# Optimization experiments

Hardware: AMD Instinct MI355X
Metric: run time of the kernel (lower is better)

## Reference

```python
import jax, jax.numpy as jnp
import numpy as np

K = 6
N_LEVELS = [200000, 50000, 12500]
CHANNELS = [3, 64, 128, 256]
DEGREE = 32
FANIN = 4          # each pooled node averages FANIN fine nodes (D values = 1/FANIN)
NUM_CLASSES = 10


def setup_inputs() -> dict:
    key = jax.random.key(0)
    ks = jax.random.split(key, 16)
    inp = {}
    inp["x"] = jax.random.normal(ks[0], (N_LEVELS[0], 3), dtype=jnp.float32)
    # random sparse connectivity per level (edge lists, COO)
    for i, n in enumerate(N_LEVELS):
        inp[f"edge_index{i}"] = jax.random.randint(ks[1 + i], (2, n * DEGREE), 0, n)
    # sparse downscale matrices: row r of D_i averages FANIN source nodes
    inp["pool_cols0"] = jax.random.randint(ks[4], (N_LEVELS[1] * FANIN,), 0, N_LEVELS[0])
    inp["pool_cols1"] = jax.random.randint(ks[5], (N_LEVELS[2] * FANIN,), 0, N_LEVELS[1])
    # ChebConv parameters: weight [K, in, out] (Glorot-ish), bias [out]
    for i in range(3):
        cin, cout = CHANNELS[i], CHANNELS[i + 1]
        scale = (2.0 / (cin + cout)) ** 0.5
        inp[f"w{i}"] = scale * jax.random.normal(ks[6 + 2 * i], (K, cin, cout), dtype=jnp.float32)
        inp[f"b{i}"] = jnp.zeros((cout,), dtype=jnp.float32)
    lin_in = N_LEVELS[-1] * CHANNELS[-1]
    inp["lw"] = jax.random.normal(ks[12], (NUM_CLASSES, lin_in), dtype=jnp.float32) * (1.0 / np.sqrt(lin_in))
    inp["lb"] = jnp.zeros((NUM_CLASSES,), dtype=jnp.float32)
    return inp


def cheb_conv(x, edge_index, weight, bias):
    """PyG ChebConv, sym normalization, lambda_max=2, unit edge weights.
    Scaled Laplacian reduces to L_hat = -D^{-1/2} A D^{-1/2} (zero diagonal)."""
    row, col = edge_index[0], edge_index[1]
    n = x.shape[0]
    w = (row != col).astype(x.dtype)                 # remove_self_loops
    deg = jax.ops.segment_sum(w, row, num_segments=n)
    dinv = jnp.where(deg > 0, jax.lax.rsqrt(deg), 0.0)
    norm = -w * dinv[row] * dinv[col]                # [E]

    def prop(h):  # scatter-add of norm * gathered source features
        return jax.ops.segment_sum(norm[:, None] * h[col], row, num_segments=n)

    Tx0 = x
    out = Tx0 @ weight[0]
    Tx1 = prop(x)
    out = out + Tx1 @ weight[1]
    for k in range(2, weight.shape[0]):
        Tx2 = 2.0 * prop(Tx1) - Tx0
        out = out + Tx2 @ weight[k]
        Tx0, Tx1 = Tx1, Tx2
    return out + bias


def pool(x, cols, n_out):
    # sparse.mm(D, x) with D having FANIN entries of 1/FANIN per row (rows sorted)
    return x[cols].reshape(n_out, FANIN, x.shape[1]).mean(axis=1)


def reference(x, edge_index0, edge_index1, edge_index2, pool_cols0, pool_cols1,
              w0, b0, w1, b1, w2, b2, lw, lb):
    h = jax.nn.relu(cheb_conv(x, edge_index0, w0, b0))
    h = pool(h, pool_cols0, N_LEVELS[1])
    h = jax.nn.relu(cheb_conv(h, edge_index1, w1, b1))
    h = pool(h, pool_cols1, N_LEVELS[2])
    h = cheb_conv(h, edge_index2, w2, b2)
    return lw @ h.reshape(-1) + lb   # F.linear on flattened features -> [num_classes]
```

## Files before the change

### kernel.cpp

```cpp
#include <hip/hip_runtime.h>
#include <hip/hip_bf16.h>


#define N0 200000
#define N1 50000
#define N2 12500
#define KCH 6
#define NCLS 10

#define SB 8
#define BROWS 256
#define BCAP 10240
#define NBUK_MAX 800
#define NBLK 1024
#define TILE_MAX 6250
#define EMAX 6400000

typedef __hip_bfloat16 bf16;
typedef _Float16 f16;
typedef f16 f16x2 __attribute__((ext_vector_type(2)));
typedef f16 f16x4 __attribute__((ext_vector_type(4)));
typedef f16 f16x8 __attribute__((ext_vector_type(8)));
typedef float f32x4 __attribute__((ext_vector_type(4)));

static __device__ __forceinline__ float b2f(bf16 v) { return __bfloat162float(v); }
static __device__ __forceinline__ float blo(unsigned u) { return __uint_as_float(u << 16); }
static __device__ __forceinline__ float bhi(unsigned u) { return __uint_as_float(u & 0xFFFF0000u); }

__global__ void detect_k(const unsigned int* __restrict__ xb, int* __restrict__ flag) {
    __shared__ int cs;
    int t = threadIdx.x;
    if (t == 0) cs = 0;
    __syncthreads();
    unsigned w = xb[t];
    unsigned e = (w >> 7) & 0xFFu;
    if (e >= 0x30u && e <= 0x43u) atomicAdd(&cs, 1);
    __syncthreads();
    if (t == 0) flag[0] = (cs < 128) ? 1 : 0;
}

__global__ __launch_bounds__(256) void convw_k(const void* __restrict__ W, f16* __restrict__ wT,
                                               int Kd, int N, const int* __restrict__ flag) {
    int isf = flag[0];
    int idx = blockIdx.x * 256 + threadIdx.x;
    if (idx >= Kd * N) return;
    int n2 = idx / Kd, k = idx - n2 * Kd;
    float v;
    if (isf) v = ((const float*)W)[(size_t)k * N + n2];
    else     v = b2f(((const bf16*)W)[(size_t)k * N + n2]);
    wT[idx] = (f16)v;
}


__global__ __launch_bounds__(256) void binH_k(const int* __restrict__ rows, const int* __restrict__ cols,
                                              int* __restrict__ cntBB, int nbuk, int E, int tile) {
    __shared__ int cnt[NBUK_MAX];
    int t = threadIdx.x;
    for (int i = t; i < nbuk; i += 256) cnt[i] = 0;
    __syncthreads();
    int beg = blockIdx.x * tile;
    int end = beg + tile;
    if (end > E) end = E;
    for (int idx = beg + t; idx < end; idx += 256) {
        int r = rows[idx], c = cols[idx];
        if (r != c) atomicAdd(&cnt[r >> SB], 1);
    }
    __syncthreads();
    for (int i = t; i < nbuk; i += 256) cntBB[(size_t)blockIdx.x * nbuk + i] = cnt[i];
}

__global__ __launch_bounds__(256) void scanBB_k(int* __restrict__ cntBB, int* __restrict__ btot, int nbuk) {
    __shared__ int ps[256];
    int b = blockIdx.x, t = threadIdx.x;
    int vals[4];
    int pt = 0;
#pragma unroll
    for (int i = 0; i < 4; ++i) { vals[i] = cntBB[(size_t)(4 * t + i) * nbuk + b]; pt += vals[i]; }
    ps[t] = pt;
    __syncthreads();
    for (int off = 1; off < 256; off <<= 1) {
        int x = (t >= off) ? ps[t - off] : 0;
        __syncthreads();
        ps[t] += x;
        __syncthreads();
    }
    int ex = ps[t] - pt;
#pragma unroll
    for (int i = 0; i < 4; ++i) { cntBB[(size_t)(4 * t + i) * nbuk + b] = ex; ex += vals[i]; }
    if (t == 255) btot[b] = ps[255];
}

__global__ __launch_bounds__(1024) void scanb_k(const int* __restrict__ btot, int* __restrict__ bbase,
                                                int nbuk, int* __restrict__ ptr, int n) {
    __shared__ int s[1024];
    int t = threadIdx.x;
    int v = (t < nbuk) ? btot[t] : 0;
    s[t] = v;
    __syncthreads();
    for (int off = 1; off < 1024; off <<= 1) {
        int x = (t >= off) ? s[t - off] : 0;
        __syncthreads();
        s[t] += x;
        __syncthreads();
    }
    if (t < nbuk) bbase[t] = s[t] - v;
    if (t == 1023) ptr[n] = s[1023];
}

__global__ __launch_bounds__(256) void binS_k(const int* __restrict__ rows, const int* __restrict__ cols,
                                              const int* __restrict__ cntBB, const int* __restrict__ bbase,
                                              unsigned* __restrict__ colB, int nbuk, int E, int tile) {
    __shared__ int lcnt[NBUK_MAX];
    __shared__ int lexc[NBUK_MAX];
    __shared__ int lfill[NBUK_MAX];
    __shared__ int gstart[NBUK_MAX];
    __shared__ int ps[256];
    __shared__ unsigned scol[TILE_MAX];
    int t = threadIdx.x;
    for (int i = t; i < nbuk; i += 256) { lcnt[i] = 0; lfill[i] = 0; }
    __syncthreads();
    int beg = blockIdx.x * tile;
    int end = beg + tile;
    if (end > E) end = E;
    for (int idx = beg + t; idx < end; idx += 256) {
        int r = rows[idx], c = cols[idx];
        if (r != c) atomicAdd(&lcnt[r >> SB], 1);
    }
    __syncthreads();
    int idx4 = 4 * t;
    int c4[4];
#pragma unroll
    for (int i = 0; i < 4; ++i) c4[i] = (idx4 + i < nbuk) ? lcnt[idx4 + i] : 0;
    int tot = c4[0] + c4[1] + c4[2] + c4[3];
    ps[t] = tot;
    __syncthreads();
    for (int off = 1; off < 256; off <<= 1) {
        int x = (t >= off) ? ps[t - off] : 0;
        __syncthreads();
        ps[t] += x;
        __syncthreads();
    }
    int run = ps[t] - tot;
#pragma unroll
    for (int i = 0; i < 4; ++i) {
        if (idx4 + i < nbuk) lexc[idx4 + i] = run;
        run += c4[i];
    }
    for (int i = t; i < nbuk; i += 256) gstart[i] = bbase[i] + cntBB[(size_t)blockIdx.x * nbuk + i];
    __syncthreads();
    for (int idx = beg + t; idx < end; idx += 256) {
        int r = rows[idx], c = cols[idx];
        if (r != c) {
            int b = r >> SB;
            int s = atomicAdd(&lfill[b], 1);
            scol[lexc[b] + s] = ((unsigned)(r & (BROWS - 1)) << 18) | (unsigned)c;
        }
    }
    __syncthreads();
    int wv = t >> 6, lane = t & 63;
    for (int b = wv; b < nbuk; b += 4) {
        int cnt2 = lcnt[b];
        int lsrc = lexc[b], gdst = gstart[b];
        for (int i = lane; i < cnt2; i += 64) colB[gdst + i] = scol[lsrc + i];
    }
}

__global__ __launch_bounds__(256) void binB_k(const int* __restrict__ btot, const int* __restrict__ bbase,
                                              const unsigned* __restrict__ colB,
                                              int* __restrict__ ptr, float* __restrict__ dinv,
                                              int* __restrict__ colS, int n) {
    __shared__ int lcnt[BROWS];
    __shared__ int lexc[BROWS];
    __shared__ int lfill[BROWS];
    __shared__ int scol[BCAP];
    int b = blockIdx.x;
    int t = threadIdx.x;
    int rowbase = b << SB;
    int rowend = rowbase + BROWS;
    if (rowend > n) rowend = n;
    int nrows = rowend - rowbase;
    int count = btot[b];
    int base = bbase[b];
    const unsigned* slab = colB + base;
    lcnt[t] = 0;
    __syncthreads();
    for (int i = t; i < count; i += 256) atomicAdd(&lcnt[slab[i] >> 18], 1);
    __syncthreads();
    int v = lcnt[t];
    lexc[t] = v;
    __syncthreads();
    for (int off = 1; off < 256; off <<= 1) {
        int x = (t >= off) ? lexc[t - off] : 0;
        __syncthreads();
        lexc[t] += x;
        __syncthreads();
    }
    int excl = lexc[t] - v;
    __syncthreads();
    lexc[t] = excl;
    __syncthreads();
    if (t < nrows) {
        ptr[rowbase + t] = base + excl;
        dinv[rowbase + t] = (v > 0) ? rsqrtf((float)v) : 0.f;
    }
    int nh = (count <= BCAP) ? 1 : 2;
    int rspan = BROWS / nh;
    for (int h = 0; h < nh; ++h) {
        int rowLo = h * rspan, rowHi = rowLo + rspan;
        int segOff = lexc[rowLo];
        int segEnd = (rowHi >= BROWS) ? count : lexc[rowHi];
        int segCnt = segEnd - segOff;
        lfill[t] = 0;
        __syncthreads();
        for (int i = t; i < count; i += 256) {
            unsigned pk = slab[i];
            int rl = pk >> 18;
            if (rl >= rowLo && rl < rowHi) {
                int s = atomicAdd(&lfill[rl], 1);
                scol[lexc[rl] + s - segOff] = (int)(pk & 0x3FFFFu);
            }
        }
        __syncthreads();
        for (int i = t; i < segCnt; i += 256) colS[base + segOff + i] = scol[i];
        __syncthreads();
    }
}


__global__ __launch_bounds__(256) void convert_x_k(const void* __restrict__ x, f16* __restrict__ Tx,
                                                   f16x4* __restrict__ G0,
                                                   const float* __restrict__ dinv, int n,
                                                   const int* __restrict__ flag) {
    int isf = flag[0];
    int r = blockIdx.x * 256 + threadIdx.x;
    if (r >= n) return;
    float v0, v1, v2;
    if (isf) {
        const float* xf = (const float*)x;
        v0 = xf[3 * r]; v1 = xf[3 * r + 1]; v2 = xf[3 * r + 2];
    } else {
        const bf16* xh = (const bf16*)x;
        v0 = b2f(xh[3 * r]); v1 = b2f(xh[3 * r + 1]); v2 = b2f(xh[3 * r + 2]);
    }
    f16x4 pk = {(f16)v0, (f16)v1, (f16)v2, (f16)dinv[r]};
    *(f16x4*)(Tx + (size_t)r * 24) = pk;
    G0[r] = pk;
}


__global__ __launch_bounds__(256) void prop_narrow_k(const int* __restrict__ ptr, const int* __restrict__ colS,
                                                     const float* __restrict__ dinv,
                                                     const f16x4* __restrict__ gin, f16x4* __restrict__ gout,
                                                     f16* __restrict__ oslot,
                                                     int n, float alpha, int useSub) {
    int wv = threadIdx.x >> 6, half = (threadIdx.x >> 5) & 1, sl = threadIdx.x & 31;
    int r = blockIdx.x * 8 + wv * 2 + half;
    if (r >= n) return;
    int s = ptr[r], e = ptr[r + 1];
    float dr = dinv[r];
    float a0 = 0.f, a1 = 0.f, a2 = 0.f;
    for (int idx = s + sl; idx < e; idx += 32) {
        int c = colS[idx];
        f16x4 h = gin[c];
        float nrm = -dr * (float)h.w;
        a0 += nrm * (float)h.x;
        a1 += nrm * (float)h.y;
        a2 += nrm * (float)h.z;
    }
#pragma unroll
    for (int off2 = 16; off2 > 0; off2 >>= 1) {
        a0 += __shfl_xor(a0, off2);
        a1 += __shfl_xor(a1, off2);
        a2 += __shfl_xor(a2, off2);
    }
    if (sl == 0) {
        float v0 = alpha * a0, v1 = alpha * a1, v2 = alpha * a2;
        if (useSub) {
            f16x4 sv = gout[r];
            v0 -= (float)sv.x; v1 -= (float)sv.y; v2 -= (float)sv.z;
        }
        f16x4 ov = {(f16)v0, (f16)v1, (f16)v2, (f16)dr};
        gout[r] = ov;
        *(f16x4*)(oslot + (size_t)r * 24) = ov;
    }
}

__global__ __launch_bounds__(256) void prop_wide2_k(const int* __restrict__ ptr, const int* __restrict__ colS,
                                                    const float* __restrict__ dinv, const f16* __restrict__ hin,
                                                    const f16* __restrict__ sub, f16* __restrict__ o,
                                                    int ld, int n, float alpha, int useSub) {
    int wv = threadIdx.x >> 6, lane = threadIdx.x & 63;
    int p = lane >> 5, q = lane & 31;
    int r = blockIdx.x * 4 + wv;
    if (r >= n) return;
    int s = ptr[r], e = ptr[r + 1];
    float dr = dinv[r];
    float ax = 0.f, ay = 0.f;
    for (int base = s; base < e; base += 64) {
        int idx = base + lane;
        int c = 0;
        float dc = 0.f;
        if (idx < e) { c = colS[idx]; dc = dinv[c]; }
        int cnt2 = e - base;
        if (cnt2 > 64) cnt2 = 64;
        int j = 0;
        for (; j + 4 <= cnt2; j += 4) {
            int j0 = j + p, j1 = j + 2 + p;
            int c0 = __shfl(c, j0), c1 = __shfl(c, j1);
            float n0 = -dr * __shfl(dc, j0), n1 = -dr * __shfl(dc, j1);
            f16x2 h0 = *(const f16x2*)(hin + (size_t)c0 * ld + 2 * q);
            f16x2 h1 = *(const f16x2*)(hin + (size_t)c1 * ld + 2 * q);
            ax += n0 * (float)h0.x + n1 * (float)h1.x;
            ay += n0 * (float)h0.y + n1 * (float)h1.y;
        }
        for (; j < cnt2; j += 2) {
            int jj = j + p;
            int valid = jj < cnt2;
            int cc = __shfl(c, valid ? jj : 0);
            float nd = __shfl(dc, valid ? jj : 0);
            float nrm = valid ? -dr * nd : 0.f;
            f16x2 h = *(const f16x2*)(hin + (size_t)cc * ld + 2 * q);
            ax += nrm * (float)h.x;
            ay += nrm * (float)h.y;
        }
    }
    ax += __shfl_xor(ax, 32);
    ay += __shfl_xor(ay, 32);
    if (p == 0) {
        size_t rb = (size_t)r * ld + 2 * q;
        float vx = alpha * ax, vy = alpha * ay;
        if (useSub) {
            f16x2 sv = *(const f16x2*)(sub + rb);
            vx -= (float)sv.x; vy -= (float)sv.y;
        }
        f16x2 ov = {(f16)vx, (f16)vy};
        *(f16x2*)(o + rb) = ov;
    }
}

__global__ __launch_bounds__(256) void prop_wide1h_k(const int* __restrict__ ptr, const int* __restrict__ colS,
                                                     const float* __restrict__ dinv, const f16* __restrict__ hin,
                                                     const f16* __restrict__ sub, f16* __restrict__ o,
                                                     int ld, int n, float alpha, int useSub) {
    int wv = threadIdx.x >> 6, lane = threadIdx.x & 63;
    int r = blockIdx.x * 4 + wv;
    if (r >= n) return;
    int s = ptr[r], e = ptr[r + 1];
    float dr = dinv[r];
    float ax = 0.f, ay = 0.f;
    for (int base = s; base < e; base += 64) {
        int idx = base + lane;
        int c = 0;
        float dc = 0.f;
        if (idx < e) { c = colS[idx]; dc = dinv[c]; }
        int cnt2 = e - base;
        if (cnt2 > 64) cnt2 = 64;
        int j = 0;
        for (; j + 4 <= cnt2; j += 4) {
            int c0 = __shfl(c, j), c1 = __shfl(c, j + 1), c2 = __shfl(c, j + 2), c3 = __shfl(c, j + 3);
            float n0 = -dr * __shfl(dc, j), n1 = -dr * __shfl(dc, j + 1);
            float n2 = -dr * __shfl(dc, j + 2), n3 = -dr * __shfl(dc, j + 3);
            f16x2 h0 = *(const f16x2*)(hin + (size_t)c0 * ld + 2 * lane);
            f16x2 h1 = *(const f16x2*)(hin + (size_t)c1 * ld + 2 * lane);
            f16x2 h2 = *(const f16x2*)(hin + (size_t)c2 * ld + 2 * lane);
            f16x2 h3 = *(const f16x2*)(hin + (size_t)c3 * ld + 2 * lane);
            ax += n0 * (float)h0.x + n1 * (float)h1.x + n2 * (float)h2.x + n3 * (float)h3.x;
            ay += n0 * (float)h0.y + n1 * (float)h1.y + n2 * (float)h2.y + n3 * (float)h3.y;
        }
        for (; j < cnt2; ++j) {
            int cc = __shfl(c, j);
            float nrm = -dr * __shfl(dc, j);
            f16x2 h = *(const f16x2*)(hin + (size_t)cc * ld + 2 * lane);
            ax += nrm * (float)h.x;
            ay += nrm * (float)h.y;
        }
    }
    size_t rb = (size_t)r * ld + 2 * lane;
    float vx = alpha * ax, vy = alpha * ay;
    if (useSub) {
        f16x2 sv = *(const f16x2*)(sub + rb);
        vx -= (float)sv.x; vy -= (float)sv.y;
    }
    f16x2 ov = {(f16)vx, (f16)vy};
    *(f16x2*)(o + rb) = ov;
}


__global__ __launch_bounds__(256) void gemm_mfma2_k(const f16* __restrict__ A, int lda,
                                                    const f16* __restrict__ WT,
                                                    const void* __restrict__ bias,
                                                    float* __restrict__ C, int M, int N, int K, int flags,
                                                    const int* __restrict__ flag) {
    __shared__ f16 As[64][40];
    __shared__ f16 Bs[64][40];
    int isf = flag[0];
    int t = threadIdx.x;
    int w = t >> 6, l = t & 63, q = l >> 4, m16 = l & 15;
    int m0 = blockIdx.y * 64, n0 = blockIdx.x * 64;
    f32x4 acc[4] = {};
    for (int k0 = 0; k0 < K; k0 += 32) {
        {
            int row = t >> 2, cg = (t & 3) * 8;
            int gm = m0 + row;
            f16x8 av = {};
            if (gm < M) av = *(const f16x8*)(A + (size_t)gm * lda + k0 + cg);
            *(f16x8*)&As[row][cg] = av;
        }
        {
            int nr = t >> 2, cg = (t & 3) * 8;
            f16x8 bv = *(const f16x8*)(WT + (size_t)(n0 + nr) * K + k0 + cg);
            *(f16x8*)&Bs[nr][cg] = bv;
        }
        __syncthreads();
        f16x8 a = *(const f16x8*)&As[w * 16 + m16][q * 8];
        f16x8 b0 = *(const f16x8*)&Bs[m16][q * 8];
        f16x8 b1 = *(const f16x8*)&Bs[16 + m16][q * 8];
        f16x8 b2 = *(const f16x8*)&Bs[32 + m16][q * 8];
        f16x8 b3 = *(const f16x8*)&Bs[48 + m16][q * 8];
        acc[0] = __builtin_amdgcn_mfma_f32_16x16x32_f16(a, b0, acc[0], 0, 0, 0);
        acc[1] = __builtin_amdgcn_mfma_f32_16x16x32_f16(a, b1, acc[1], 0, 0, 0);
        acc[2] = __builtin_amdgcn_mfma_f32_16x16x32_f16(a, b2, acc[2], 0, 0, 0);
        acc[3] = __builtin_amdgcn_mfma_f32_16x16x32_f16(a, b3, acc[3], 0, 0, 0);
        __syncthreads();
    }
#pragma unroll
    for (int tile = 0; tile < 4; ++tile) {
        int gn = n0 + tile * 16 + m16;
        float bv = 0.f;
        if (flags & 4) {
            if (isf) bv = ((const float*)bias)[gn];
            else     bv = b2f(((const bf16*)bias)[gn]);
        }
#pragma unroll
        for (int i = 0; i < 4; ++i) {
            int gm = m0 + w * 16 + q * 4 + i;
            if (gm < M) {
                float v = acc[tile][i] + bv;
                if (flags & 1) v = fmaxf(v, 0.f);
                C[(size_t)gm * N + gn] = v;
            }
        }
    }
}


__global__ __launch_bounds__(256) void gemm_k(const f16* __restrict__ A, int lda,
                                              const void* __restrict__ W,
                                              const void* __restrict__ bias,
                                              float* __restrict__ C, int M, int N, int K, int flags,
                                              const int* __restrict__ flag) {
    __shared__ float As[16][65];
    __shared__ float Ws[16][64];
    int isf = flag[0];
    int pack3 = flags & 8;
    int t = threadIdx.x;
    int tn = t & 15, tm = t >> 4;
    int m0 = blockIdx.y * 64, n0 = blockIdx.x * 64;
    float acc[4][4] = {};
    for (int k0 = 0; k0 < K; k0 += 16) {
#pragma unroll
        for (int i = 0; i < 4; ++i) {
            int idx = i * 256 + t;
            int m = idx >> 4, k = idx & 15;
            int gm = m0 + m, gk = k0 + k;
            int phys = pack3 ? (gk + gk / 3) : gk;
            As[k][m] = (gm < M && gk < K) ? (float)A[(size_t)gm * lda + phys] : 0.f;
        }
        if (isf) {
            const float* Wf = (const float*)W;
#pragma unroll
            for (int i = 0; i < 4; ++i) {
                int idx = i * 256 + t;
                int k = idx >> 6, nn = idx & 63;
                int gk = k0 + k;
                Ws[k][nn] = (gk < K) ? Wf[(size_t)gk * N + n0 + nn] : 0.f;
            }
        } else {
            const bf16* Wh = (const bf16*)W;
#pragma unroll
            for (int i = 0; i < 4; ++i) {
                int idx = i * 256 + t;
                int k = idx >> 6, nn = idx & 63;
                int gk = k0 + k;
                Ws[k][nn] = (gk < K) ? b2f(Wh[(size_t)gk * N + n0 + nn]) : 0.f;
            }
        }
        __syncthreads();
#pragma unroll
        for (int kk = 0; kk < 16; ++kk) {
            float a[4], b[4];
#pragma unroll
            for (int i = 0; i < 4; ++i) a[i] = As[kk][tm * 4 + i];
#pragma unroll
            for (int j = 0; j < 4; ++j) b[j] = Ws[kk][tn * 4 + j];
#pragma unroll
            for (int i = 0; i < 4; ++i)
#pragma unroll
                for (int j = 0; j < 4; ++j) acc[i][j] += a[i] * b[j];
        }
        __syncthreads();
    }
#pragma unroll
    for (int i = 0; i < 4; ++i) {
        int gm = m0 + tm * 4 + i;
        if (gm >= M) continue;
#pragma unroll
        for (int j = 0; j < 4; ++j) {
            int gn = n0 + tn * 4 + j;
            size_t ci = (size_t)gm * N + gn;
            float v = acc[i][j];
            if (flags & 4) {
                if (isf) v += ((const float*)bias)[gn];
                else     v += b2f(((const bf16*)bias)[gn]);
            }
            if (flags & 1) v = fmaxf(v, 0.f);
            C[ci] = v;
        }
    }
}


__global__ __launch_bounds__(256) void pool_k(const float* __restrict__ in, const int* __restrict__ pcols,
                                              f16* __restrict__ out, int n_out, int C, int ld) {
    int idx = blockIdx.x * 256 + threadIdx.x;
    if (idx >= n_out * C) return;
    int r = idx / C, ch = idx - r * C;
    const int* pc = pcols + (size_t)r * 4;
    float ssum = 0.f;
#pragma unroll
    for (int f = 0; f < 4; ++f) ssum += in[(size_t)pc[f] * C + ch];
    out[(size_t)r * ld + ch] = (f16)(0.25f * ssum);
}


__global__ __launch_bounds__(256) void linear10b_k(const float* __restrict__ h, const void* __restrict__ lw,
                                                   float* __restrict__ accum, int LIN, const int* __restrict__ flag) {
    int isf = flag[0];
    int t = threadIdx.x;
    int nvec = LIN >> 3;
    int stride = gridDim.x * 256;
    float p[NCLS];
#pragma unroll
    for (int c = 0; c < NCLS; ++c) p[c] = 0.f;
    const float4* h4 = (const float4*)h;
    if (isf) {
        const float4* lw4 = (const float4*)lw;
        size_t ro = (size_t)(LIN >> 2);
        for (int i = blockIdx.x * 256 + t; i < nvec; i += stride) {
            float4 a0 = h4[2 * i], a1 = h4[2 * i + 1];
#pragma unroll
            for (int c = 0; c < NCLS; ++c) {
                float4 b0v = lw4[c * ro + 2 * i], b1v = lw4[c * ro + 2 * i + 1];
                p[c] += a0.x * b0v.x + a0.y * b0v.y + a0.z * b0v.z + a0.w * b0v.w
                      + a1.x * b1v.x + a1.y * b1v.y + a1.z * b1v.z + a1.w * b1v.w;
            }
        }
    } else {
        const uint4* lwv = (const uint4*)lw;
        size_t ro = (size_t)nvec;
        for (int i = blockIdx.x * 256 + t; i < nvec; i += stride) {
            float4 a0 = h4[2 * i], a1 = h4[2 * i + 1];
#pragma unroll
            for (int c = 0; c < NCLS; ++c) {
                uint4 w4 = lwv[c * ro + i];
                p[c] += a0.x * blo(w4.x) + a0.y * bhi(w4.x)
                      + a0.z * blo(w4.y) + a0.w * bhi(w4.y)
                      + a1.x * blo(w4.z) + a1.y * bhi(w4.z)
                      + a1.z * blo(w4.w) + a1.w * bhi(w4.w);
            }
        }
    }
    __shared__ float wsum[4][NCLS];
    int wv = t >> 6, lane = t & 63;
#pragma unroll
    for (int c = 0; c < NCLS; ++c) {
        float v = p[c];
        for (int off2 = 32; off2 > 0; off2 >>= 1) v += __shfl_down(v, off2);
        if (lane == 0) wsum[wv][c] = v;
    }
    __syncthreads();
    if (t < NCLS) {
        float s = wsum[0][t] + wsum[1][t] + wsum[2][t] + wsum[3][t];
        unsafeAtomicAdd(&accum[t], s);
    }
}

__global__ void finalize_k(const float* __restrict__ accum, const void* __restrict__ lb,
                           void* __restrict__ outp, const int* __restrict__ flag) {
    int isf = flag[0];
    int t = threadIdx.x;
    if (t < NCLS) {
        float lbv;
        if (isf) lbv = ((const float*)lb)[t];
        else     lbv = b2f(((const bf16*)lb)[t]);
        float v = accum[t] + lbv;
        if (isf) ((float*)outp)[t] = v;
        else     ((bf16*)outp)[t] = __float2bfloat16(v);
    }
}

__global__ void diag_k(void* __restrict__ outp, float val, const int* __restrict__ flag) {
    int isf = flag[0];
    int t = threadIdx.x;
    if (t < NCLS) {
        if (isf) ((float*)outp)[t] = val;
        else     ((bf16*)outp)[t] = __float2bfloat16(val);
    }
}


extern "C" void kernel_launch(void* const* d_in, const int* in_sizes, int n_in,
                              void* d_out, int out_size, void* d_ws, size_t ws_size,
                              hipStream_t stream) {
    const void* x  = d_in[0];
    const int* ei0 = (const int*)d_in[1];
    const int* ei1 = (const int*)d_in[2];
    const int* ei2 = (const int*)d_in[3];
    const int* pc0 = (const int*)d_in[4];
    const int* pc1 = (const int*)d_in[5];
    const void* w0 = d_in[6];
    const void* b0 = d_in[7];
    const void* w1 = d_in[8];
    const void* b1 = d_in[9];
    const void* w2 = d_in[10];
    const void* b2 = d_in[11];
    const void* lw = d_in[12];
    const void* lb = d_in[13];

    const int E0 = in_sizes[1] / 2, E1 = in_sizes[2] / 2, E2 = in_sizes[3] / 2;

    char* base = (char*)d_ws;
    size_t off = 0;
    auto alloc = [&](size_t bytes) -> void* {
        void* p = base + off;
        off += (bytes + 255) & ~(size_t)255;
        return p;
    };
    f16*      TxAll = (f16*)alloc((size_t)19200000 * 2);
    float*    OutB  = (float*)alloc((size_t)12800000 * 4);
    int*      colS  = (int*)alloc((size_t)EMAX * 4);
    unsigned* colB  = (unsigned*)alloc((size_t)EMAX * 4);
    int*      cntBB = (int*)alloc((size_t)NBLK * NBUK_MAX * 4);
    f16x4*    G0    = (f16x4*)alloc((size_t)N0 * 8);
    f16x4*    G1    = (f16x4*)alloc((size_t)N0 * 8);
    int*      ptr   = (int*)alloc((size_t)(N0 + 1) * 4);
    float*    dinv  = (float*)alloc((size_t)N0 * 4);
    int*      btot  = (int*)alloc((size_t)NBUK_MAX * 4);
    int*      bbase = (int*)alloc((size_t)NBUK_MAX * 4);
    f16*      wT1   = (f16*)alloc((size_t)384 * 128 * 2);
    f16*      wT2   = (f16*)alloc((size_t)768 * 256 * 2);
    float*    accum = (float*)alloc(64);
    int*      flag  = (int*)(accum + 16);

    detect_k<<<1, 256, 0, stream>>>((const unsigned int*)x, flag);

    const size_t NEED = 158000000;
    if (ws_size < NEED) {
        diag_k<<<1, 64, 0, stream>>>(d_out, (float)(ws_size >> 20), flag);
        return;
    }

    convw_k<<<(384 * 128 + 255) / 256, 256, 0, stream>>>(w1, wT1, 384, 128, flag);
    convw_k<<<(768 * 256 + 255) / 256, 256, 0, stream>>>(w2, wT2, 768, 256, flag);

    struct Lvl {
        int n, E, cin, cout;
        const int *rows, *cols;
        const void *w, *b;
        int relu;
    };
    Lvl L[3] = {
        {N0, E0, 3, 64, ei0, ei0 + E0, w0, b0, 1},
        {N1, E1, 64, 128, ei1, ei1 + E1, w1, b1, 1},
        {N2, E2, 128, 256, ei2, ei2 + E2, w2, b2, 0},
    };
    f16x4* G[2] = {G0, G1};

    for (int li = 0; li < 3; ++li) {
        const Lvl& v = L[li];
        int n = v.n, E = v.E, cin = v.cin, cout = v.cout;
        int nbuk = (n + BROWS - 1) >> SB;
        int tile = (E + NBLK - 1) / NBLK;
        int ld = (li == 0) ? 24 : KCH * cin;
        int slot = (li == 0) ? 4 : cin;

        binH_k<<<NBLK, 256, 0, stream>>>(v.rows, v.cols, cntBB, nbuk, E, tile);
        scanBB_k<<<nbuk, 256, 0, stream>>>(cntBB, btot, nbuk);
        scanb_k<<<1, 1024, 0, stream>>>(btot, bbase, nbuk, ptr, n);
        binS_k<<<NBLK, 256, 0, stream>>>(v.rows, v.cols, cntBB, bbase, colB, nbuk, E, tile);
        binB_k<<<nbuk, 256, 0, stream>>>(btot, bbase, colB, ptr, dinv, colS, n);

        if (li == 0)
            convert_x_k<<<(N0 + 255) / 256, 256, 0, stream>>>(x, TxAll, G0, dinv, N0, flag);

        for (int k = 1; k < KCH; ++k) {
            float alpha = (k >= 2) ? 2.f : 1.f;
            if (li == 0) {
                prop_narrow_k<<<(n + 7) / 8, 256, 0, stream>>>(ptr, colS, dinv,
                                                               G[(k - 1) & 1], G[k & 1],
                                                               TxAll + (size_t)k * 4, n, alpha, k >= 2);
            } else {
                const f16* hin = TxAll + (size_t)(k - 1) * slot;
                const f16* sub = (k >= 2) ? (TxAll + (size_t)(k - 2) * slot) : nullptr;
                f16* o = TxAll + (size_t)k * slot;
                if (cin == 64)
                    prop_wide2_k<<<(n + 3) / 4, 256, 0, stream>>>(ptr, colS, dinv, hin, sub, o, ld, n, alpha, k >= 2);
                else
                    prop_wide1h_k<<<(n + 3) / 4, 256, 0, stream>>>(ptr, colS, dinv, hin, sub, o, ld, n, alpha, k >= 2);
            }
        }

        dim3 gg(cout / 64, (n + 63) / 64);
        if (li == 0)
            gemm_k<<<gg, 256, 0, stream>>>(TxAll, ld, v.w, v.b, OutB, n, cout, KCH * cin, 4 | 8 | (v.relu ? 1 : 0), flag);
        else
            gemm_mfma2_k<<<gg, 256, 0, stream>>>(TxAll, ld, (li == 1) ? wT1 : wT2, v.b, OutB, n, cout, KCH * cin,
                                                 4 | (v.relu ? 1 : 0), flag);

        if (li == 0)
            pool_k<<<(N1 * 64 + 255) / 256, 256, 0, stream>>>(OutB, pc0, TxAll, N1, 64, KCH * 64);
        else if (li == 1)
            pool_k<<<(N2 * 128 + 255) / 256, 256, 0, stream>>>(OutB, pc1, TxAll, N2, 128, KCH * 128);
    }

    hipMemsetAsync(accum, 0, 64, stream);
    {
        dim3 lg(512);
        linear10b_k<<<lg, 256, 0, stream>>>(OutB, lw, accum, N2 * 256, flag);
    }
    finalize_k<<<1, 64, 0, stream>>>(accum, lb, d_out, flag);
}
```

Baseline: 1.055 ms.

## Batch CSR construction for all three levels and store pre-pool GEMM output as f16

The per-level binning, scan and sort kernels are merged into single launches that cover all three graph levels at once, each with its own buffers. The x conversion moves into the bucket-sort kernel, the accumulator memset moves into the scan, and the two weight-transpose kernels become one launch. The GEMM outputs for levels 0 and 1 are written as f16 and pooled with 4-wide vector loads, which halves that traffic. The cost is more workspace and a small precision loss on the intermediate activations.

```diff
diff --git a/kernel.cpp b/kernel.cpp
--- a/kernel.cpp
+++ b/kernel.cpp
@@ -14,7 +14,6 @@
 #define NBUK_MAX 800
 #define NBLK 1024
 #define TILE_MAX 6250
-#define EMAX 6400000
 
 typedef __hip_bfloat16 bf16;
 typedef _Float16 f16;
@@ -27,6 +26,13 @@
 static __device__ __forceinline__ float blo(unsigned u) { return __uint_as_float(u << 16); }
 static __device__ __forceinline__ float bhi(unsigned u) { return __uint_as_float(u & 0xFFFF0000u); }
 
+struct BLvl {
+    const int* rows; const int* cols;
+    int* cntBB; int* btot; int* bbase;
+    unsigned* colB; int* colS; int* ptr; float* dinv;
+    int E, nbuk, tile, n;
+};
+
 __global__ void detect_k(const unsigned int* __restrict__ xb, int* __restrict__ flag) {
     __shared__ int cs;
     int t = threadIdx.x;
@@ -39,43 +45,58 @@
     if (t == 0) flag[0] = (cs < 128) ? 1 : 0;
 }
 
-__global__ __launch_bounds__(256) void convw_k(const void* __restrict__ W, f16* __restrict__ wT,
-                                               int Kd, int N, const int* __restrict__ flag) {
+__global__ __launch_bounds__(256) void convw2_k(const void* __restrict__ W1, f16* __restrict__ wT1,
+                                                const void* __restrict__ W2, f16* __restrict__ wT2,
+                                                const int* __restrict__ flag) {
     int isf = flag[0];
     int idx = blockIdx.x * 256 + threadIdx.x;
-    if (idx >= Kd * N) return;
-    int n2 = idx / Kd, k = idx - n2 * Kd;
-    float v;
-    if (isf) v = ((const float*)W)[(size_t)k * N + n2];
-    else     v = b2f(((const bf16*)W)[(size_t)k * N + n2]);
-    wT[idx] = (f16)v;
-}
-
-
-__global__ __launch_bounds__(256) void binH_k(const int* __restrict__ rows, const int* __restrict__ cols,
-                                              int* __restrict__ cntBB, int nbuk, int E, int tile) {
+    const int tot1 = 384 * 128;
+    const int tot2 = 768 * 256;
+    if (idx < tot1) {
+        int n2 = idx / 384, k = idx - n2 * 384;
+        float v;
+        if (isf) v = ((const float*)W1)[(size_t)k * 128 + n2];
+        else     v = b2f(((const bf16*)W1)[(size_t)k * 128 + n2]);
+        wT1[idx] = (f16)v;
+    } else if (idx < tot1 + tot2) {
+        int i2 = idx - tot1;
+        int n2 = i2 / 768, k = i2 - n2 * 768;
+        float v;
+        if (isf) v = ((const float*)W2)[(size_t)k * 256 + n2];
+        else     v = b2f(((const bf16*)W2)[(size_t)k * 256 + n2]);
+        wT2[i2] = (f16)v;
+    }
+}
+
+
+__global__ __launch_bounds__(256) void binH3_k(BLvl a, BLvl b, BLvl c) {
+    BLvl lv = (blockIdx.y == 0) ? a : ((blockIdx.y == 1) ? b : c);
     __shared__ int cnt[NBUK_MAX];
     int t = threadIdx.x;
-    for (int i = t; i < nbuk; i += 256) cnt[i] = 0;
-    __syncthreads();
-    int beg = blockIdx.x * tile;
-    int end = beg + tile;
-    if (end > E) end = E;
+    for (int i = t; i < lv.nbuk; i += 256) cnt[i] = 0;
+    __syncthreads();
+    int beg = blockIdx.x * lv.tile;
+    int end = beg + lv.tile;
+    if (end > lv.E) end = lv.E;
     for (int idx = beg + t; idx < end; idx += 256) {
-        int r = rows[idx], c = cols[idx];
-        if (r != c) atomicAdd(&cnt[r >> SB], 1);
-    }
-    __syncthreads();
-    for (int i = t; i < nbuk; i += 256) cntBB[(size_t)blockIdx.x * nbuk + i] = cnt[i];
-}
-
-__global__ __launch_bounds__(256) void scanBB_k(int* __restrict__ cntBB, int* __restrict__ btot, int nbuk) {
+        int r = lv.rows[idx], cc = lv.cols[idx];
+        if (r != cc) atomicAdd(&cnt[r >> SB], 1);
+    }
+    __syncthreads();
+    for (int i = t; i < lv.nbuk; i += 256) lv.cntBB[(size_t)blockIdx.x * lv.nbuk + i] = cnt[i];
+}
+
+__global__ __launch_bounds__(256) void scanBB3_k(BLvl a, BLvl b, BLvl c) {
     __shared__ int ps[256];
-    int b = blockIdx.x, t = threadIdx.x;
+    int gb = blockIdx.x, t = threadIdx.x;
+    BLvl lv; int b0;
+    if (gb < a.nbuk) { lv = a; b0 = gb; }
+    else if (gb < a.nbuk + b.nbuk) { lv = b; b0 = gb - a.nbuk; }
+    else { lv = c; b0 = gb - a.nbuk - b.nbuk; }
     int vals[4];
     int pt = 0;
 #pragma unroll
-    for (int i = 0; i < 4; ++i) { vals[i] = cntBB[(size_t)(4 * t + i) * nbuk + b]; pt += vals[i]; }
+    for (int i = 0; i < 4; ++i) { vals[i] = lv.cntBB[(size_t)(4 * t + i) * lv.nbuk + b0]; pt += vals[i]; }
     ps[t] = pt;
     __syncthreads();
     for (int off = 1; off < 256; off <<= 1) {
@@ -86,15 +107,16 @@
     }
     int ex = ps[t] - pt;
 #pragma unroll
-    for (int i = 0; i < 4; ++i) { cntBB[(size_t)(4 * t + i) * nbuk + b] = ex; ex += vals[i]; }
-    if (t == 255) btot[b] = ps[255];
-}
-
-__global__ __launch_bounds__(1024) void scanb_k(const int* __restrict__ btot, int* __restrict__ bbase,
-                                                int nbuk, int* __restrict__ ptr, int n) {
+    for (int i = 0; i < 4; ++i) { lv.cntBB[(size_t)(4 * t + i) * lv.nbuk + b0] = ex; ex += vals[i]; }
+    if (t == 255) lv.btot[b0] = ps[255];
+}
+
+__global__ __launch_bounds__(1024) void scanb3_k(BLvl a, BLvl b, BLvl c, float* __restrict__ accum) {
     __shared__ int s[1024];
-    int t = threadIdx.x;
-    int v = (t < nbuk) ? btot[t] : 0;
+    BLvl lv = (blockIdx.x == 0) ? a : ((blockIdx.x == 1) ? b : c);
+    int t = threadIdx.x;
+    if (blockIdx.x == 0 && t < 16) accum[t] = 0.f;
+    int v = (t < lv.nbuk) ? lv.btot[t] : 0;
     s[t] = v;
     __syncthreads();
     for (int off = 1; off < 1024; off <<= 1) {
@@ -103,13 +125,12 @@
         s[t] += x;
         __syncthreads();
     }
-    if (t < nbuk) bbase[t] = s[t] - v;
-    if (t == 1023) ptr[n] = s[1023];
-}
-
-__global__ __launch_bounds__(256) void binS_k(const int* __restrict__ rows, const int* __restrict__ cols,
-                                              const int* __restrict__ cntBB, const int* __restrict__ bbase,
-                                              unsigned* __restrict__ colB, int nbuk, int E, int tile) {
+    if (t < lv.nbuk) lv.bbase[t] = s[t] - v;
+    if (t == 1023) lv.ptr[lv.n] = s[1023];
+}
+
+__global__ __launch_bounds__(256) void binS3_k(BLvl a, BLvl b, BLvl c) {
+    BLvl lv = (blockIdx.y == 0) ? a : ((blockIdx.y == 1) ? b : c);
     __shared__ int lcnt[NBUK_MAX];
     __shared__ int lexc[NBUK_MAX];
     __shared__ int lfill[NBUK_MAX];
@@ -117,20 +138,20 @@
     __shared__ int ps[256];
     __shared__ unsigned scol[TILE_MAX];
     int t = threadIdx.x;
-    for (int i = t; i < nbuk; i += 256) { lcnt[i] = 0; lfill[i] = 0; }
-    __syncthreads();
-    int beg = blockIdx.x * tile;
-    int end = beg + tile;
-    if (end > E) end = E;
+    for (int i = t; i < lv.nbuk; i += 256) { lcnt[i] = 0; lfill[i] = 0; }
+    __syncthreads();
+    int beg = blockIdx.x * lv.tile;
+    int end = beg + lv.tile;
+    if (end > lv.E) end = lv.E;
     for (int idx = beg + t; idx < end; idx += 256) {
-        int r = rows[idx], c = cols[idx];
-        if (r != c) atomicAdd(&lcnt[r >> SB], 1);
+        int r = lv.rows[idx], cc = lv.cols[idx];
+        if (r != cc) atomicAdd(&lcnt[r >> SB], 1);
     }
     __syncthreads();
     int idx4 = 4 * t;
     int c4[4];
 #pragma unroll
-    for (int i = 0; i < 4; ++i) c4[i] = (idx4 + i < nbuk) ? lcnt[idx4 + i] : 0;
+    for (int i = 0; i < 4; ++i) c4[i] = (idx4 + i < lv.nbuk) ? lcnt[idx4 + i] : 0;
     int tot = c4[0] + c4[1] + c4[2] + c4[3];
     ps[t] = tot;
     __syncthreads();
@@ -143,45 +164,48 @@
     int run = ps[t] - tot;
 #pragma unroll
     for (int i = 0; i < 4; ++i) {
-        if (idx4 + i < nbuk) lexc[idx4 + i] = run;
+        if (idx4 + i < lv.nbuk) lexc[idx4 + i] = run;
         run += c4[i];
     }
-    for (int i = t; i < nbuk; i += 256) gstart[i] = bbase[i] + cntBB[(size_t)blockIdx.x * nbuk + i];
+    for (int i = t; i < lv.nbuk; i += 256) gstart[i] = lv.bbase[i] + lv.cntBB[(size_t)blockIdx.x * lv.nbuk + i];
     __syncthreads();
     for (int idx = beg + t; idx < end; idx += 256) {
-        int r = rows[idx], c = cols[idx];
-        if (r != c) {
-            int b = r >> SB;
-            int s = atomicAdd(&lfill[b], 1);
-            scol[lexc[b] + s] = ((unsigned)(r & (BROWS - 1)) << 18) | (unsigned)c;
+        int r = lv.rows[idx], cc = lv.cols[idx];
+        if (r != cc) {
+            int bk = r >> SB;
+            int s = atomicAdd(&lfill[bk], 1);
+            scol[lexc[bk] + s] = ((unsigned)(r & (BROWS - 1)) << 18) | (unsigned)cc;
         }
     }
     __syncthreads();
     int wv = t >> 6, lane = t & 63;
-    for (int b = wv; b < nbuk; b += 4) {
-        int cnt2 = lcnt[b];
-        int lsrc = lexc[b], gdst = gstart[b];
-        for (int i = lane; i < cnt2; i += 64) colB[gdst + i] = scol[lsrc + i];
-    }
-}
-
-__global__ __launch_bounds__(256) void binB_k(const int* __restrict__ btot, const int* __restrict__ bbase,
-                                              const unsigned* __restrict__ colB,
-                                              int* __restrict__ ptr, float* __restrict__ dinv,
-                                              int* __restrict__ colS, int n) {
+    for (int bk = wv; bk < lv.nbuk; bk += 4) {
+        int cnt2 = lcnt[bk];
+        int lsrc = lexc[bk], gdst = gstart[bk];
+        for (int i = lane; i < cnt2; i += 64) lv.colB[gdst + i] = scol[lsrc + i];
+    }
+}
+
+__global__ __launch_bounds__(256) void binB3_k(BLvl a, BLvl b, BLvl c,
+                                               const void* __restrict__ x, f16* __restrict__ TxAll,
+                                               f16x4* __restrict__ G0, const int* __restrict__ flag) {
     __shared__ int lcnt[BROWS];
     __shared__ int lexc[BROWS];
     __shared__ int lfill[BROWS];
     __shared__ int scol[BCAP];
-    int b = blockIdx.x;
-    int t = threadIdx.x;
-    int rowbase = b << SB;
+    int gb = blockIdx.x;
+    int t = threadIdx.x;
+    BLvl lv; int b0, lvl;
+    if (gb < a.nbuk) { lv = a; b0 = gb; lvl = 0; }
+    else if (gb < a.nbuk + b.nbuk) { lv = b; b0 = gb - a.nbuk; lvl = 1; }
+    else { lv = c; b0 = gb - a.nbuk - b.nbuk; lvl = 2; }
+    int rowbase = b0 << SB;
     int rowend = rowbase + BROWS;
-    if (rowend > n) rowend = n;
+    if (rowend > lv.n) rowend = lv.n;
     int nrows = rowend - rowbase;
-    int count = btot[b];
-    int base = bbase[b];
-    const unsigned* slab = colB + base;
+    int count = lv.btot[b0];
+    int base = lv.bbase[b0];
+    const unsigned* slab = lv.colB + base;
     lcnt[t] = 0;
     __syncthreads();
     for (int i = t; i < count; i += 256) atomicAdd(&lcnt[slab[i] >> 18], 1);
@@ -190,9 +214,9 @@
     lexc[t] = v;
     __syncthreads();
     for (int off = 1; off < 256; off <<= 1) {
-        int x = (t >= off) ? lexc[t - off] : 0;
-        __syncthreads();
-        lexc[t] += x;
+        int xx = (t >= off) ? lexc[t - off] : 0;
+        __syncthreads();
+        lexc[t] += xx;
         __syncthreads();
     }
     int excl = lexc[t] - v;
@@ -200,8 +224,24 @@
     lexc[t] = excl;
     __syncthreads();
     if (t < nrows) {
-        ptr[rowbase + t] = base + excl;
-        dinv[rowbase + t] = (v > 0) ? rsqrtf((float)v) : 0.f;
+        lv.ptr[rowbase + t] = base + excl;
+        float dr = (v > 0) ? rsqrtf((float)v) : 0.f;
+        lv.dinv[rowbase + t] = dr;
+        if (lvl == 0) {
+            int r = rowbase + t;
+            int isf = flag[0];
+            float v0, v1, v2;
+            if (isf) {
+                const float* xf = (const float*)x;
+                v0 = xf[3 * r]; v1 = xf[3 * r + 1]; v2 = xf[3 * r + 2];
+            } else {
+                const bf16* xh = (const bf16*)x;
+                v0 = b2f(xh[3 * r]); v1 = b2f(xh[3 * r + 1]); v2 = b2f(xh[3 * r + 2]);
+            }
+            f16x4 pk = {(f16)v0, (f16)v1, (f16)v2, (f16)dr};
+            *(f16x4*)(TxAll + (size_t)r * 24) = pk;
+            G0[r] = pk;
+        }
     }
     int nh = (count <= BCAP) ? 1 : 2;
     int rspan = BROWS / nh;
@@ -221,30 +261,9 @@
             }
         }
         __syncthreads();
-        for (int i = t; i < segCnt; i += 256) colS[base + segOff + i] = scol[i];
-        __syncthreads();
-    }
-}
-
-
-__global__ __launch_bounds__(256) void convert_x_k(const void* __restrict__ x, f16* __restrict__ Tx,
-                                                   f16x4* __restrict__ G0,
-                                                   const float* __restrict__ dinv, int n,
-                                                   const int* __restrict__ flag) {
-    int isf = flag[0];
-    int r = blockIdx.x * 256 + threadIdx.x;
-    if (r >= n) return;
-    float v0, v1, v2;
-    if (isf) {
-        const float* xf = (const float*)x;
-        v0 = xf[3 * r]; v1 = xf[3 * r + 1]; v2 = xf[3 * r + 2];
-    } else {
-        const bf16* xh = (const bf16*)x;
-        v0 = b2f(xh[3 * r]); v1 = b2f(xh[3 * r + 1]); v2 = b2f(xh[3 * r + 2]);
-    }
-    f16x4 pk = {(f16)v0, (f16)v1, (f16)v2, (f16)dinv[r]};
-    *(f16x4*)(Tx + (size_t)r * 24) = pk;
-    G0[r] = pk;
+        for (int i = t; i < segCnt; i += 256) lv.colS[base + segOff + i] = scol[i];
+        __syncthreads();
+    }
 }
 
 
@@ -389,7 +408,7 @@
 __global__ __launch_bounds__(256) void gemm_mfma2_k(const f16* __restrict__ A, int lda,
                                                     const f16* __restrict__ WT,
                                                     const void* __restrict__ bias,
-                                                    float* __restrict__ C, int M, int N, int K, int flags,
+                                                    void* __restrict__ C, int M, int N, int K, int flags,
                                                     const int* __restrict__ flag) {
     __shared__ f16 As[64][40];
     __shared__ f16 Bs[64][40];
@@ -412,15 +431,15 @@
             *(f16x8*)&Bs[nr][cg] = bv;
         }
         __syncthreads();
-        f16x8 a = *(const f16x8*)&As[w * 16 + m16][q * 8];
+        f16x8 aa = *(const f16x8*)&As[w * 16 + m16][q * 8];
         f16x8 b0 = *(const f16x8*)&Bs[m16][q * 8];
         f16x8 b1 = *(const f16x8*)&Bs[16 + m16][q * 8];
         f16x8 b2 = *(const f16x8*)&Bs[32 + m16][q * 8];
         f16x8 b3 = *(const f16x8*)&Bs[48 + m16][q * 8];
-        acc[0] = __builtin_amdgcn_mfma_f32_16x16x32_f16(a, b0, acc[0], 0, 0, 0);
-        acc[1] = __builtin_amdgcn_mfma_f32_16x16x32_f16(a, b1, acc[1], 0, 0, 0);
-        acc[2] = __builtin_amdgcn_mfma_f32_16x16x32_f16(a, b2, acc[2], 0, 0, 0);
-        acc[3] = __builtin_amdgcn_mfma_f32_16x16x32_f16(a, b3, acc[3], 0, 0, 0);
+        acc[0] = __builtin_amdgcn_mfma_f32_16x16x32_f16(aa, b0, acc[0], 0, 0, 0);
+        acc[1] = __builtin_amdgcn_mfma_f32_16x16x32_f16(aa, b1, acc[1], 0, 0, 0);
+        acc[2] = __builtin_amdgcn_mfma_f32_16x16x32_f16(aa, b2, acc[2], 0, 0, 0);
+        acc[3] = __builtin_amdgcn_mfma_f32_16x16x32_f16(aa, b3, acc[3], 0, 0, 0);
         __syncthreads();
     }
 #pragma unroll
@@ -437,7 +456,9 @@
             if (gm < M) {
                 float v = acc[tile][i] + bv;
                 if (flags & 1) v = fmaxf(v, 0.f);
-                C[(size_t)gm * N + gn] = v;
+                size_t ci = (size_t)gm * N + gn;
+                if (flags & 16) ((f16*)C)[ci] = (f16)v;
+                else            ((float*)C)[ci] = v;
             }
         }
     }
@@ -447,7 +468,7 @@
 __global__ __launch_bounds__(256) void gemm_k(const f16* __restrict__ A, int lda,
                                               const void* __restrict__ W,
                                               const void* __restrict__ bias,
-                                              float* __restrict__ C, int M, int N, int K, int flags,
+                                              void* __restrict__ C, int M, int N, int K, int flags,
                                               const int* __restrict__ flag) {
     __shared__ float As[16][65];
     __shared__ float Ws[16][64];
@@ -488,15 +509,15 @@
         __syncthreads();
 #pragma unroll
         for (int kk = 0; kk < 16; ++kk) {
-            float a[4], b[4];
-#pragma unroll
-            for (int i = 0; i < 4; ++i) a[i] = As[kk][tm * 4 + i];
-#pragma unroll
-            for (int j = 0; j < 4; ++j) b[j] = Ws[kk][tn * 4 + j];
+            float aa[4], bb[4];
+#pragma unroll
+            for (int i = 0; i < 4; ++i) aa[i] = As[kk][tm * 4 + i];
+#pragma unroll
+            for (int j = 0; j < 4; ++j) bb[j] = Ws[kk][tn * 4 + j];
 #pragma unroll
             for (int i = 0; i < 4; ++i)
 #pragma unroll
-                for (int j = 0; j < 4; ++j) acc[i][j] += a[i] * b[j];
+                for (int j = 0; j < 4; ++j) acc[i][j] += aa[i] * bb[j];
         }
         __syncthreads();
     }
@@ -514,22 +535,28 @@
                 else     v += b2f(((const bf16*)bias)[gn]);
             }
             if (flags & 1) v = fmaxf(v, 0.f);
-            C[ci] = v;
-        }
-    }
-}
-
-
-__global__ __launch_bounds__(256) void pool_k(const float* __restrict__ in, const int* __restrict__ pcols,
+            if (flags & 16) ((f16*)C)[ci] = (f16)v;
+            else            ((float*)C)[ci] = v;
+        }
+    }
+}
+
+
+__global__ __launch_bounds__(256) void pool_k(const f16* __restrict__ in, const int* __restrict__ pcols,
                                               f16* __restrict__ out, int n_out, int C, int ld) {
     int idx = blockIdx.x * 256 + threadIdx.x;
-    if (idx >= n_out * C) return;
-    int r = idx / C, ch = idx - r * C;
+    int C4 = C >> 2;
+    if (idx >= n_out * C4) return;
+    int r = idx / C4, c4 = (idx - r * C4) * 4;
     const int* pc = pcols + (size_t)r * 4;
-    float ssum = 0.f;
-#pragma unroll
-    for (int f = 0; f < 4; ++f) ssum += in[(size_t)pc[f] * C + ch];
-    out[(size_t)r * ld + ch] = (f16)(0.25f * ssum);
+    float s0 = 0.f, s1 = 0.f, s2 = 0.f, s3 = 0.f;
+#pragma unroll
+    for (int f = 0; f < 4; ++f) {
+        f16x4 v = *(const f16x4*)(in + (size_t)pc[f] * C + c4);
+        s0 += (float)v.x; s1 += (float)v.y; s2 += (float)v.z; s3 += (float)v.w;
+    }
+    f16x4 o = {(f16)(0.25f * s0), (f16)(0.25f * s1), (f16)(0.25f * s2), (f16)(0.25f * s3)};
+    *(f16x4*)(out + (size_t)r * ld + c4) = o;
 }
 
 
@@ -628,6 +655,8 @@
     const void* lb = d_in[13];
 
     const int E0 = in_sizes[1] / 2, E1 = in_sizes[2] / 2, E2 = in_sizes[3] / 2;
+    const int Ns[3] = {N0, N1, N2};
+    const int Es[3] = {E0, E1, E2};
 
     char* base = (char*)d_ws;
     size_t off = 0;
@@ -638,60 +667,69 @@
     };
     f16*      TxAll = (f16*)alloc((size_t)19200000 * 2);
     float*    OutB  = (float*)alloc((size_t)12800000 * 4);
-    int*      colS  = (int*)alloc((size_t)EMAX * 4);
-    unsigned* colB  = (unsigned*)alloc((size_t)EMAX * 4);
-    int*      cntBB = (int*)alloc((size_t)NBLK * NBUK_MAX * 4);
+    f16*      OutBh = (f16*)OutB;
     f16x4*    G0    = (f16x4*)alloc((size_t)N0 * 8);
     f16x4*    G1    = (f16x4*)alloc((size_t)N0 * 8);
-    int*      ptr   = (int*)alloc((size_t)(N0 + 1) * 4);
-    float*    dinv  = (float*)alloc((size_t)N0 * 4);
-    int*      btot  = (int*)alloc((size_t)NBUK_MAX * 4);
-    int*      bbase = (int*)alloc((size_t)NBUK_MAX * 4);
     f16*      wT1   = (f16*)alloc((size_t)384 * 128 * 2);
     f16*      wT2   = (f16*)alloc((size_t)768 * 256 * 2);
     float*    accum = (float*)alloc(64);
     int*      flag  = (int*)(accum + 16);
 
+    BLvl BL[3];
+    for (int i = 0; i < 3; ++i) {
+        int n = Ns[i], E = Es[i];
+        BL[i].nbuk = (n + BROWS - 1) >> SB;
+        BL[i].tile = (E + NBLK - 1) / NBLK;
+        BL[i].E = E;
+        BL[i].n = n;
+        BL[i].cntBB = (int*)alloc((size_t)NBLK * BL[i].nbuk * 4);
+        BL[i].btot  = (int*)alloc((size_t)BL[i].nbuk * 4);
+        BL[i].bbase = (int*)alloc((size_t)BL[i].nbuk * 4);
+        BL[i].colB  = (unsigned*)alloc((size_t)E * 4);
+        BL[i].colS  = (int*)alloc((size_t)E * 4);
+        BL[i].ptr   = (int*)alloc((size_t)(n + 1) * 4);
+        BL[i].dinv  = (float*)alloc((size_t)n * 4);
+    }
+    BL[0].rows = ei0; BL[0].cols = ei0 + E0;
+    BL[1].rows = ei1; BL[1].cols = ei1 + E1;
+    BL[2].rows = ei2; BL[2].cols = ei2 + E2;
+
     detect_k<<<1, 256, 0, stream>>>((const unsigned int*)x, flag);
 
-    const size_t NEED = 158000000;
-    if (ws_size < NEED) {
+    if (ws_size < off) {
         diag_k<<<1, 64, 0, stream>>>(d_out, (float)(ws_size >> 20), flag);
         return;
     }
 
-    convw_k<<<(384 * 128 + 255) / 256, 256, 0, stream>>>(w1, wT1, 384, 128, flag);
-    convw_k<<<(768 * 256 + 255) / 256, 256, 0, stream>>>(w2, wT2, 768, 256, flag);
+    convw2_k<<<(384 * 128 + 768 * 256 + 255) / 256, 256, 0, stream>>>(w1, wT1, w2, wT2, flag);
+
+    int nbukT = BL[0].nbuk + BL[1].nbuk + BL[2].nbuk;
+    binH3_k<<<dim3(NBLK, 3), 256, 0, stream>>>(BL[0], BL[1], BL[2]);
+    scanBB3_k<<<nbukT, 256, 0, stream>>>(BL[0], BL[1], BL[2]);
+    scanb3_k<<<3, 1024, 0, stream>>>(BL[0], BL[1], BL[2], accum);
+    binS3_k<<<dim3(NBLK, 3), 256, 0, stream>>>(BL[0], BL[1], BL[2]);
+    binB3_k<<<nbukT, 256, 0, stream>>>(BL[0], BL[1], BL[2], x, TxAll, G0, flag);
 
     struct Lvl {
-        int n, E, cin, cout;
-        const int *rows, *cols;
+        int n, cin, cout;
         const void *w, *b;
         int relu;
     };
     Lvl L[3] = {
-        {N0, E0, 3, 64, ei0, ei0 + E0, w0, b0, 1},
-        {N1, E1, 64, 128, ei1, ei1 + E1, w1, b1, 1},
-        {N2, E2, 128, 256, ei2, ei2 + E2, w2, b2, 0},
+        {N0, 3, 64, w0, b0, 1},
+        {N1, 64, 128, w1, b1, 1},
+        {N2, 128, 256, w2, b2, 0},
     };
     f16x4* G[2] = {G0, G1};
 
     for (int li = 0; li < 3; ++li) {
         const Lvl& v = L[li];
-        int n = v.n, E = v.E, cin = v.cin, cout = v.cout;
-        int nbuk = (n + BROWS - 1) >> SB;
-        int tile = (E + NBLK - 1) / NBLK;
+        int n = v.n, cin = v.cin, cout = v.cout;
         int ld = (li == 0) ? 24 : KCH * cin;
         int slot = (li == 0) ? 4 : cin;
-
-        binH_k<<<NBLK, 256, 0, stream>>>(v.rows, v.cols, cntBB, nbuk, E, tile);
-        scanBB_k<<<nbuk, 256, 0, stream>>>(cntBB, btot, nbuk);
-        scanb_k<<<1, 1024, 0, stream>>>(btot, bbase, nbuk, ptr, n);
-        binS_k<<<NBLK, 256, 0, stream>>>(v.rows, v.cols, cntBB, bbase, colB, nbuk, E, tile);
-        binB_k<<<nbuk, 256, 0, stream>>>(btot, bbase, colB, ptr, dinv, colS, n);
-
-        if (li == 0)
-            convert_x_k<<<(N0 + 255) / 256, 256, 0, stream>>>(x, TxAll, G0, dinv, N0, flag);
+        const int* ptr = BL[li].ptr;
+        const int* colS = BL[li].colS;
+        const float* dinv = BL[li].dinv;
 
         for (int k = 1; k < KCH; ++k) {
             float alpha = (k >= 2) ? 2.f : 1.f;
@@ -711,19 +749,20 @@
         }
 
         dim3 gg(cout / 64, (n + 63) / 64);
+        int f16out = (li < 2) ? 16 : 0;
         if (li == 0)
-            gemm_k<<<gg, 256, 0, stream>>>(TxAll, ld, v.w, v.b, OutB, n, cout, KCH * cin, 4 | 8 | (v.relu ? 1 : 0), flag);
+            gemm_k<<<gg, 256, 0, stream>>>(TxAll, ld, v.w, v.b, OutB, n, cout, KCH * cin,
+                                           4 | 8 | f16out | (v.relu ? 1 : 0), flag);
         else
             gemm_mfma2_k<<<gg, 256, 0, stream>>>(TxAll, ld, (li == 1) ? wT1 : wT2, v.b, OutB, n, cout, KCH * cin,
-                                                 4 | (v.relu ? 1 : 0), flag);
+                                                 4 | f16out | (v.relu ? 1 : 0), flag);
 
         if (li == 0)
-            pool_k<<<(N1 * 64 + 255) / 256, 256, 0, stream>>>(OutB, pc0, TxAll, N1, 64, KCH * 64);
+            pool_k<<<(N1 * 16 + 255) / 256, 256, 0, stream>>>(OutBh, pc0, TxAll, N1, 64, KCH * 64);
         else if (li == 1)
-            pool_k<<<(N2 * 128 + 255) / 256, 256, 0, stream>>>(OutB, pc1, TxAll, N2, 128, KCH * 128);
-    }
-
-    hipMemsetAsync(accum, 0, 64, stream);
+            pool_k<<<(N2 * 32 + 255) / 256, 256, 0, stream>>>(OutBh, pc1, TxAll, N2, 128, KCH * 128);
+    }
+
     {
         dim3 lg(512);
         linear10b_k<<<lg, 256, 0, stream>>>(OutB, lw, accum, N2 * 256, flag);
```

Result: faster. 971.4 us (-7.9%).
